# Optimization experiments

Hardware: AMD Instinct MI355X
Metric: run time of the kernel (lower is better)

Reference implementation:

```python
import jax, jax.numpy as jnp
import numpy as np

B, GEO_CH, SEM_CH, H, W = 8, 256, 256, 64, 64
HS, WS = 32, 32  # semantic branch spatial size
EPS_ATTN = 1e-6
EPS_GN = 1e-5


def _phi(x):
    return jax.nn.elu(x) + 1.0


def setup_inputs() -> dict:
    key = jax.random.key(0)
    ks = jax.random.split(key, 8)
    f_geo = jax.random.normal(ks[0], (B, GEO_CH, H, W), dtype=jnp.float32)
    f_sem = jax.random.normal(ks[1], (B, SEM_CH, HS, WS), dtype=jnp.float32)
    s = 0.02
    Wq = jax.random.normal(ks[2], (SEM_CH, GEO_CH), dtype=jnp.float32) * s
    Wk = jax.random.normal(ks[3], (SEM_CH, SEM_CH), dtype=jnp.float32) * s
    Wv = jax.random.normal(ks[4], (SEM_CH, SEM_CH), dtype=jnp.float32) * s
    Wo = jax.random.normal(ks[5], (GEO_CH, SEM_CH), dtype=jnp.float32) * s
    bq = jnp.zeros((SEM_CH,), jnp.float32)
    bk = jnp.zeros((SEM_CH,), jnp.float32)
    bv = jnp.zeros((SEM_CH,), jnp.float32)
    bo = jnp.zeros((GEO_CH,), jnp.float32)
    gn_w = jnp.ones((GEO_CH,), jnp.float32)
    gn_b = jnp.zeros((GEO_CH,), jnp.float32)
    return {"f_geo": f_geo, "f_sem": f_sem, "Wq": Wq, "bq": bq, "Wk": Wk,
            "bk": bk, "Wv": Wv, "bv": bv, "Wo": Wo, "bo": bo,
            "gn_w": gn_w, "gn_b": gn_b}


def _conv1x1(x, Wm, b):
    # x: [B,Cin,H,W], Wm: [Cout,Cin] -> [B,Cout,H,W]
    return jnp.einsum('oc,bchw->bohw', Wm, x) + b[None, :, None, None]


def reference(f_geo, f_sem, Wq, bq, Wk, bk, Wv, bv, Wo, bo, gn_w, gn_b):
    b, cg, h, w = f_geo.shape
    n = h * w
    # bilinear resize, half-pixel centers == torch align_corners=False
    f_sem_r = jax.image.resize(f_sem, (b, f_sem.shape[1], h, w), method='bilinear')
    Q = _phi(_conv1x1(f_geo, Wq, bq)).reshape(b, -1, n)      # [B,Cs,N]
    K = _phi(_conv1x1(f_sem_r, Wk, bk)).reshape(b, -1, n)    # [B,Cs,N]
    V = _conv1x1(f_sem_r, Wv, bv).reshape(b, -1, n)          # [B,Cs,N]
    KV = jnp.einsum('bcn,bdn->bcd', K, V)                    # [B,Cs,Cs]
    QKV = jnp.einsum('bcn,bcd->bnd', Q, KV)                  # [B,N,Cs]
    K_sum = K.sum(axis=-1)                                   # [B,Cs]
    norm = jnp.einsum('bcn,bc->bn', Q, K_sum)[..., None] + EPS_ATTN  # [B,N,1]
    out = (QKV / norm).transpose(0, 2, 1).reshape(b, -1, h, w)
    y = f_geo + _conv1x1(out, Wo, bo)
    # GroupNorm(1, geo_ch): normalize over (C,H,W) per sample, per-channel affine
    mu = y.mean(axis=(1, 2, 3), keepdims=True)
    var = y.var(axis=(1, 2, 3), keepdims=True)
    yn = (y - mu) * jax.lax.rsqrt(var + EPS_GN)
    return yn * gn_w[None, :, None, None] + gn_b[None, :, None, None]
```

## Files before the change

### kernel.cpp

```cpp
#include <hip/hip_runtime.h>
#include <hip/hip_bf16.h>


#define B_ 8
#define C_ 256
#define N_ 4096
#define NS_ 1024
#define KVCH 16

typedef unsigned short u16;
using bf16x8 = __attribute__((ext_vector_type(8))) short;
using f32x4 = __attribute__((ext_vector_type(4))) float;

__device__ inline u16 f2bf(float f) {
  unsigned u = __builtin_bit_cast(unsigned, f);
  unsigned r = (u + 0x7fffu + ((u >> 16) & 1u)) >> 16;
  return (u16)r;
}
__device__ inline float bf2f(u16 x) {
  return __builtin_bit_cast(float, ((unsigned)x) << 16);
}

__device__ __forceinline__ void gl_lds16(const u16* g, u16* l) {
  __builtin_amdgcn_global_load_lds((const __attribute__((address_space(1))) void*)g,
                                   (__attribute__((address_space(3))) void*)l, 16, 0, 0);
}

__device__ inline void gemm128_nt(const u16* __restrict__ At, const u16* __restrict__ Bt,
                                  int lda, int ldb, int k0, int k1,
                                  u16* __restrict__ lds, f32x4 acc[4][4])
{
  const int t = threadIdx.x;
  const int lane = t & 63, wave = t >> 6;
  const int wr = wave >> 1, wc = wave & 1;
  const int lr = lane & 15, lg = lane >> 4;
  const int sr = t >> 2, skv = (t & 3) * 8;
  u16* Ab = lds;
  u16* Bb = lds + 128 * 32;
  const u16* gA0 = At + (size_t)sr * lda + skv;
  const u16* gA1 = At + (size_t)(sr + 64) * lda + skv;
  const u16* gB0 = Bt + (size_t)sr * ldb + skv;
  const u16* gB1 = Bt + (size_t)(sr + 64) * ldb + skv;
  u16* dA0 = Ab + wave * 512;
  u16* dA1 = Ab + 2048 + wave * 512;
  u16* dB0 = Bb + wave * 512;
  u16* dB1 = Bb + 2048 + wave * 512;
  const u16* ap = Ab + (wr * 64 + lr) * 32 + lg * 8;
  const u16* bp = Bb + (wc * 64 + lr) * 32 + lg * 8;
  for (int k = k0; k < k1; k += 32) {
    gl_lds16(gA0 + k, dA0);
    gl_lds16(gA1 + k, dA1);
    gl_lds16(gB0 + k, dB0);
    gl_lds16(gB1 + k, dB1);
    __syncthreads();
    bf16x8 af[4], bfr[4];
#pragma unroll
    for (int i = 0; i < 4; ++i) af[i] = *reinterpret_cast<const bf16x8*>(ap + i * 16 * 32);
#pragma unroll
    for (int i = 0; i < 4; ++i) bfr[i] = *reinterpret_cast<const bf16x8*>(bp + i * 16 * 32);
#pragma unroll
    for (int m = 0; m < 4; ++m)
#pragma unroll
      for (int n = 0; n < 4; ++n)
        acc[m][n] = __builtin_amdgcn_mfma_f32_16x16x32_bf16(af[m], bfr[n], acc[m][n], 0, 0, 0);
    __syncthreads();
  }
}

__device__ inline void zero_acc(f32x4 acc[4][4]) {
#pragma unroll
  for (int m = 0; m < 4; ++m)
#pragma unroll
    for (int n = 0; n < 4; ++n)
#pragma unroll
      for (int r = 0; r < 4; ++r) acc[m][n][r] = 0.f;
}

__device__ inline void ep_stage_half(const f32x4 acc[4][4], float* eplds, int h,
                                     int wr, int wc, int lr, int lg)
{
  if (wr == h) {
#pragma unroll
    for (int m = 0; m < 4; ++m)
#pragma unroll
      for (int n = 0; n < 4; ++n)
#pragma unroll
        for (int r = 0; r < 4; ++r)
          eplds[(m * 16 + lg * 4 + r) * 132 + wc * 64 + n * 16 + lr] = acc[m][n][r];
  }
}

__global__ __launch_bounds__(256) void k_transpose_cast(const float* __restrict__ in,
                                                        u16* __restrict__ out, int rows, int cols)
{
  __shared__ float tile[32][33];
  int b = blockIdx.z;
  const float* src = in + (size_t)b * rows * cols;
  u16* dst = out + (size_t)b * rows * cols;
  int c0 = blockIdx.x * 32, r0 = blockIdx.y * 32;
  int tx = threadIdx.x & 31, ty = threadIdx.x >> 5;
#pragma unroll
  for (int i = 0; i < 32; i += 8)
    tile[ty + i][tx] = src[(size_t)(r0 + ty + i) * cols + (c0 + tx)];
  __syncthreads();
#pragma unroll
  for (int i = 0; i < 32; i += 8)
    dst[(size_t)(c0 + ty + i) * rows + (r0 + tx)] = f2bf(tile[tx][ty + i]);
}

__global__ __launch_bounds__(256) void k_cast4(const float* __restrict__ w0, const float* __restrict__ w1,
                                               const float* __restrict__ w2, const float* __restrict__ w3,
                                               u16* o0, u16* o1, u16* o2, u16* o3,
                                               float* __restrict__ stats, float* __restrict__ normv)
{
  int i = blockIdx.x * 256 + threadIdx.x;
  o0[i] = f2bf(w0[i]); o1[i] = f2bf(w1[i]); o2[i] = f2bf(w2[i]); o3[i] = f2bf(w3[i]);
  if (i < 16) stats[i] = 0.f;
  if (i < B_ * N_) normv[i] = 1e-6f;
}

__global__ __launch_bounds__(256) void k_semconv(const u16* __restrict__ fsemT,
                                                 const u16* __restrict__ Wk, const u16* __restrict__ Wv,
                                                 const float* __restrict__ bk, const float* __restrict__ bv,
                                                 u16* __restrict__ Kpre, u16* __restrict__ Vpre)
{
  __shared__ u16 glds[2 * 128 * 32];
  __shared__ float eplds[64 * 132];
  int b = blockIdx.z >> 1, sel = blockIdx.z & 1;
  int m0 = blockIdx.y * 128, n0 = blockIdx.x * 128;
  const u16* A = (sel ? Wv : Wk) + (size_t)m0 * C_;
  const u16* Bm = fsemT + (size_t)b * NS_ * C_ + (size_t)n0 * C_;
  const float* bias = sel ? bv : bk;
  u16* out = (sel ? Vpre : Kpre) + (size_t)b * C_ * NS_;
  f32x4 acc[4][4];
  zero_acc(acc);
  gemm128_nt(A, Bm, C_, C_, 0, C_, glds, acc);
  int t = threadIdx.x, lane = t & 63, wave = t >> 6;
  int wr = wave >> 1, wc = wave & 1, lr = lane & 15, lg = lane >> 4;
  for (int h = 0; h < 2; ++h) {
    __syncthreads();
    ep_stage_half(acc, eplds, h, wr, wc, lr, lg);
    __syncthreads();
#pragma unroll
    for (int it = 0; it < 8; ++it) {
      int rloc = it * 8 + (t >> 5), cloc = (t & 31) * 4;
      int row = m0 + h * 64 + rloc;
      float4 a = *(const float4*)&eplds[rloc * 132 + cloc];
      float bi = bias[row];
      ushort4 o;
      o.x = f2bf(a.x + bi); o.y = f2bf(a.y + bi); o.z = f2bf(a.z + bi); o.w = f2bf(a.w + bi);
      *(ushort4*)&out[(size_t)row * NS_ + n0 + cloc] = o;
    }
  }
}

__global__ __launch_bounds__(256) void k_resize(const u16* __restrict__ Kpre, const u16* __restrict__ Vpre,
                                                u16* __restrict__ Kbf, u16* __restrict__ Vbf,
                                                float* __restrict__ Ksum)
{
  int sel = blockIdx.y;
  const u16* src = (sel ? Vpre : Kpre) + (size_t)blockIdx.x * NS_;
  u16* dst = (sel ? Vbf : Kbf) + (size_t)blockIdx.x * N_;
  float s = 0.f;
  for (int i = threadIdx.x; i < N_; i += 256) {
    int yy = i >> 6, xx = i & 63;
    int yh = yy >> 1, xh = xx >> 1;
    int ys0, ys1, xs0, xs1; float wy0, wy1, wx0, wx1;
    if (yy & 1) { ys0 = yh; ys1 = yh < 31 ? yh + 1 : 31; wy0 = 0.75f; wy1 = 0.25f; }
    else        { ys0 = yh > 0 ? yh - 1 : 0; ys1 = yh;   wy0 = 0.25f; wy1 = 0.75f; }
    if (xx & 1) { xs0 = xh; xs1 = xh < 31 ? xh + 1 : 31; wx0 = 0.75f; wx1 = 0.25f; }
    else        { xs0 = xh > 0 ? xh - 1 : 0; xs1 = xh;   wx0 = 0.25f; wx1 = 0.75f; }
    float r0 = wx0 * bf2f(src[ys0 * 32 + xs0]) + wx1 * bf2f(src[ys0 * 32 + xs1]);
    float r1 = wx0 * bf2f(src[ys1 * 32 + xs0]) + wx1 * bf2f(src[ys1 * 32 + xs1]);
    float v = wy0 * r0 + wy1 * r1;
    if (!sel) { v = v > 0.f ? v + 1.f : __expf(v); s += v; }
    dst[i] = f2bf(v);
  }
  if (!sel) {
    __shared__ float red[256];
    red[threadIdx.x] = s; __syncthreads();
    for (int off = 128; off > 0; off >>= 1) {
      if (threadIdx.x < off) red[threadIdx.x] += red[threadIdx.x + off];
      __syncthreads();
    }
    if (threadIdx.x == 0) Ksum[blockIdx.x] = red[0];
  }
}

__global__ __launch_bounds__(256) void k_kv(const u16* __restrict__ Kbf, const u16* __restrict__ Vbf,
                                            float* __restrict__ KVpart)
{
  __shared__ u16 glds[2 * 128 * 32];
  __shared__ float eplds[64 * 132];
  int tn = blockIdx.x, tm = blockIdx.y;
  int b = blockIdx.z >> 4, ch = blockIdx.z & 15;
  const int kspan = N_ / KVCH;
  const u16* A = Kbf + (size_t)b * C_ * N_ + (size_t)tm * 128 * N_;
  const u16* Bm = Vbf + (size_t)b * C_ * N_ + (size_t)tn * 128 * N_;
  f32x4 acc[4][4];
  zero_acc(acc);
  gemm128_nt(A, Bm, N_, N_, ch * kspan, ch * kspan + kspan, glds, acc);
  float* out = KVpart + ((size_t)(b * KVCH + ch) * 4 + tm * 2 + tn) * (128 * 128);
  int t = threadIdx.x, lane = t & 63, wave = t >> 6;
  int wr = wave >> 1, wc = wave & 1, lr = lane & 15, lg = lane >> 4;
  for (int h = 0; h < 2; ++h) {
    __syncthreads();
    ep_stage_half(acc, eplds, h, wr, wc, lr, lg);
    __syncthreads();
#pragma unroll
    for (int it = 0; it < 8; ++it) {
      int rloc = it * 8 + (t >> 5), cloc = (t & 31) * 4;
      float4 a = *(const float4*)&eplds[rloc * 132 + cloc];
      *(float4*)&out[(size_t)(h * 64 + rloc) * 128 + cloc] = a;
    }
  }
}

__global__ __launch_bounds__(256) void k_kvred(const float* __restrict__ KVpart, u16* __restrict__ KVbf)
{
  int idx = blockIdx.x * 256 + threadIdx.x;
  int b = idx >> 16, cd = idx & 65535;
  int c = cd >> 8, d = cd & 255;
  int tile = (c >> 7) * 2 + (d >> 7);
  int loc = (c & 127) * 128 + (d & 127);
  float s = 0.f;
#pragma unroll
  for (int ch = 0; ch < KVCH; ++ch)
    s += KVpart[((size_t)(b * KVCH + ch) * 4 + tile) * 16384 + loc];
  KVbf[idx] = f2bf(s);
}

__global__ __launch_bounds__(256) void k_mgemm(const u16* __restrict__ Wo, const u16* __restrict__ KVbf,
                                               u16* __restrict__ Mbf)
{
  __shared__ u16 glds[2 * 128 * 32];
  __shared__ float eplds[64 * 132];
  int tn = blockIdx.x, tm = blockIdx.y, b = blockIdx.z;
  const u16* A = Wo + (size_t)tm * 128 * C_;
  const u16* Bm = KVbf + (size_t)b * C_ * C_ + (size_t)tn * 128 * C_;
  f32x4 acc[4][4];
  zero_acc(acc);
  gemm128_nt(A, Bm, C_, C_, 0, C_, glds, acc);
  u16* out = Mbf + (size_t)b * C_ * C_;
  int t = threadIdx.x, lane = t & 63, wave = t >> 6;
  int wr = wave >> 1, wc = wave & 1, lr = lane & 15, lg = lane >> 4;
  for (int h = 0; h < 2; ++h) {
    __syncthreads();
    ep_stage_half(acc, eplds, h, wr, wc, lr, lg);
    __syncthreads();
#pragma unroll
    for (int it = 0; it < 8; ++it) {
      int rloc = it * 8 + (t >> 5), cloc = (t & 31) * 4;
      int row = tm * 128 + h * 64 + rloc;
      float4 a = *(const float4*)&eplds[rloc * 132 + cloc];
      ushort4 o;
      o.x = f2bf(a.x); o.y = f2bf(a.y); o.z = f2bf(a.z); o.w = f2bf(a.w);
      *(ushort4*)&out[(size_t)row * C_ + tn * 128 + cloc] = o;
    }
  }
}

__global__ __launch_bounds__(256) void k_qgemm(const u16* __restrict__ fgeoT, const u16* __restrict__ Wq,
                                               const float* __restrict__ bq, const float* __restrict__ Ksum,
                                               u16* __restrict__ Qt, float* __restrict__ normv)
{
  __shared__ u16 glds[2 * 128 * 32];
  __shared__ float eplds[64 * 132];
  int tc = blockIdx.x, tn = blockIdx.y, b = blockIdx.z;
  const u16* A = fgeoT + (size_t)b * N_ * C_ + (size_t)tn * 128 * C_;
  const u16* Bm = Wq + (size_t)tc * 128 * C_;
  f32x4 acc[4][4];
  zero_acc(acc);
  gemm128_nt(A, Bm, C_, C_, 0, C_, glds, acc);
  u16* out = Qt + (size_t)b * N_ * C_;
  float* nb = normv + (size_t)b * N_;
  int t = threadIdx.x, lane = t & 63, wave = t >> 6;
  int wr = wave >> 1, wc = wave & 1, lr = lane & 15, lg = lane >> 4;
  for (int h = 0; h < 2; ++h) {
    __syncthreads();
    ep_stage_half(acc, eplds, h, wr, wc, lr, lg);
    __syncthreads();
#pragma unroll
    for (int it = 0; it < 8; ++it) {
      int rloc = it * 8 + (t >> 5), cloc = (t & 31) * 4;
      int row = tn * 128 + h * 64 + rloc;
      int col = tc * 128 + cloc;
      float4 a = *(const float4*)&eplds[rloc * 132 + cloc];
      float4 bqv = *(const float4*)&bq[col];
      float4 ks = *(const float4*)&Ksum[b * C_ + col];
      float v0 = a.x + bqv.x; v0 = v0 > 0.f ? v0 + 1.f : __expf(v0);
      float v1 = a.y + bqv.y; v1 = v1 > 0.f ? v1 + 1.f : __expf(v1);
      float v2 = a.z + bqv.z; v2 = v2 > 0.f ? v2 + 1.f : __expf(v2);
      float v3 = a.w + bqv.w; v3 = v3 > 0.f ? v3 + 1.f : __expf(v3);
      ushort4 o;
      o.x = f2bf(v0); o.y = f2bf(v1); o.z = f2bf(v2); o.w = f2bf(v3);
      *(ushort4*)&out[(size_t)row * C_ + col] = o;
      float p = v0 * ks.x + v1 * ks.y + v2 * ks.z + v3 * ks.w;
      p += __shfl_xor(p, 1); p += __shfl_xor(p, 2);
      p += __shfl_xor(p, 4); p += __shfl_xor(p, 8); p += __shfl_xor(p, 16);
      if ((t & 31) == 0) atomicAdd(&nb[row], p);
    }
  }
}

__global__ __launch_bounds__(256) void k_final(const u16* __restrict__ Mbf, const u16* __restrict__ Qt,
                                               const float* __restrict__ fgeo, const float* __restrict__ bo,
                                               const float* __restrict__ normv,
                                               float* __restrict__ y, float* __restrict__ stats)
{
  __shared__ u16 glds[2 * 128 * 32];
  __shared__ float eplds[64 * 132];
  int tn = blockIdx.x, tm = blockIdx.y, b = blockIdx.z;
  const u16* A = Mbf + (size_t)b * C_ * C_ + (size_t)tm * 128 * C_;
  const u16* Bm = Qt + (size_t)b * N_ * C_ + (size_t)tn * 128 * C_;
  f32x4 acc[4][4];
  zero_acc(acc);
  gemm128_nt(A, Bm, C_, C_, 0, C_, glds, acc);
  const float* nrm = normv + (size_t)b * N_;
  const float* fg = fgeo + (size_t)b * C_ * N_;
  float* yb = y + (size_t)b * C_ * N_;
  int t = threadIdx.x, lane = t & 63, wave = t >> 6;
  int wr = wave >> 1, wc = wave & 1, lr = lane & 15, lg = lane >> 4;
  float ssum = 0.f, ssq = 0.f;
  for (int h = 0; h < 2; ++h) {
    __syncthreads();
    ep_stage_half(acc, eplds, h, wr, wc, lr, lg);
    __syncthreads();
#pragma unroll
    for (int it = 0; it < 8; ++it) {
      int rloc = it * 8 + (t >> 5), cloc = (t & 31) * 4;
      int row = tm * 128 + h * 64 + rloc;
      int col = tn * 128 + cloc;
      float4 a = *(const float4*)&eplds[rloc * 132 + cloc];
      float4 nv = *(const float4*)&nrm[col];
      float4 f = *(const float4*)&fg[(size_t)row * N_ + col];
      float bov = bo[row];
      float4 v;
      v.x = f.x + bov + a.x / nv.x;
      v.y = f.y + bov + a.y / nv.y;
      v.z = f.z + bov + a.z / nv.z;
      v.w = f.w + bov + a.w / nv.w;
      *(float4*)&yb[(size_t)row * N_ + col] = v;
      ssum += v.x + v.y + v.z + v.w;
      ssq += v.x * v.x + v.y * v.y + v.z * v.z + v.w * v.w;
    }
  }
#pragma unroll
  for (int off = 1; off < 64; off <<= 1) {
    ssum += __shfl_xor(ssum, off);
    ssq += __shfl_xor(ssq, off);
  }
  if (lane == 0) {
    atomicAdd(&stats[b * 2], ssum);
    atomicAdd(&stats[b * 2 + 1], ssq);
  }
}

__global__ __launch_bounds__(256) void k_gn(float* __restrict__ y, const float* __restrict__ stats,
                                            const float* __restrict__ gnw, const float* __restrict__ gnb)
{
  int idx = blockIdx.x * 256 + threadIdx.x;
  int elem = idx * 8;
  int b = elem >> 20;
  int o = (elem >> 12) & 255;
  const float cnt = (float)C_ * (float)N_;
  float mu = stats[b * 2] / cnt;
  float var = stats[b * 2 + 1] / cnt - mu * mu;
  float rs = rsqrtf(var + 1e-5f);
  float sc = gnw[o] * rs;
  float sh = gnb[o] - mu * sc;
  float4* p = reinterpret_cast<float4*>(y) + idx * 2;
  float4 v0 = p[0], v1 = p[1];
  v0.x = v0.x * sc + sh; v0.y = v0.y * sc + sh; v0.z = v0.z * sc + sh; v0.w = v0.w * sc + sh;
  v1.x = v1.x * sc + sh; v1.y = v1.y * sc + sh; v1.z = v1.z * sc + sh; v1.w = v1.w * sc + sh;
  p[0] = v0; p[1] = v1;
}

extern "C" void kernel_launch(void* const* d_in, const int* in_sizes, int n_in,
                              void* d_out, int out_size, void* d_ws, size_t ws_size,
                              hipStream_t stream)
{
  const float* f_geo = (const float*)d_in[0];
  const float* f_sem = (const float*)d_in[1];
  const float* Wq = (const float*)d_in[2];
  const float* bq = (const float*)d_in[3];
  const float* Wk = (const float*)d_in[4];
  const float* bk = (const float*)d_in[5];
  const float* Wv = (const float*)d_in[6];
  const float* bv = (const float*)d_in[7];
  const float* Wo = (const float*)d_in[8];
  const float* bo = (const float*)d_in[9];
  const float* gnw = (const float*)d_in[10];
  const float* gnb = (const float*)d_in[11];
  float* y = (float*)d_out;

  char* w = (char*)d_ws;
  auto alloc = [&](size_t bytes) { char* p = w; w += (bytes + 255) & ~(size_t)255; return p; };
  u16* fsemT = (u16*)alloc((size_t)B_ * NS_ * C_ * 2);
  u16* fgeoT = (u16*)alloc((size_t)B_ * N_ * C_ * 2);
  u16* Wqb = (u16*)alloc(65536 * 2);
  u16* Wkb = (u16*)alloc(65536 * 2);
  u16* Wvb = (u16*)alloc(65536 * 2);
  u16* Wob = (u16*)alloc(65536 * 2);
  u16* Kpre = (u16*)alloc((size_t)B_ * C_ * NS_ * 2);
  u16* Vpre = (u16*)alloc((size_t)B_ * C_ * NS_ * 2);
  u16* Kbf = (u16*)alloc((size_t)B_ * C_ * N_ * 2);
  u16* Vbf = (u16*)alloc((size_t)B_ * C_ * N_ * 2);
  float* Ksum = (float*)alloc((size_t)B_ * C_ * 4);
  float* KVpart = (float*)alloc((size_t)B_ * KVCH * 4 * 16384 * 4);
  u16* KVbf = (u16*)alloc((size_t)B_ * C_ * C_ * 2);
  u16* Mbf = (u16*)alloc((size_t)B_ * C_ * C_ * 2);
  u16* Qt = (u16*)alloc((size_t)B_ * N_ * C_ * 2);
  float* normv = (float*)alloc((size_t)B_ * N_ * 4);
  float* stats = (float*)alloc(256);

  k_transpose_cast<<<dim3(NS_ / 32, C_ / 32, B_), 256, 0, stream>>>(f_sem, fsemT, C_, NS_);
  k_transpose_cast<<<dim3(N_ / 32, C_ / 32, B_), 256, 0, stream>>>(f_geo, fgeoT, C_, N_);
  k_cast4<<<dim3(256), 256, 0, stream>>>(Wq, Wk, Wv, Wo, Wqb, Wkb, Wvb, Wob, stats, normv);
  k_semconv<<<dim3(8, 2, 16), 256, 0, stream>>>(fsemT, Wkb, Wvb, bk, bv, Kpre, Vpre);
  k_resize<<<dim3(B_ * C_, 2), 256, 0, stream>>>(Kpre, Vpre, Kbf, Vbf, Ksum);
  k_kv<<<dim3(2, 2, B_ * KVCH), 256, 0, stream>>>(Kbf, Vbf, KVpart);
  k_kvred<<<dim3(2048), 256, 0, stream>>>(KVpart, KVbf);
  k_mgemm<<<dim3(2, 2, B_), 256, 0, stream>>>(Wob, KVbf, Mbf);
  k_qgemm<<<dim3(2, 32, B_), 256, 0, stream>>>(fgeoT, Wqb, bq, Ksum, Qt, normv);
  k_final<<<dim3(32, 2, B_), 256, 0, stream>>>(Mbf, Qt, f_geo, bo, normv, y, stats);
  k_gn<<<dim3(B_ * C_ * N_ / 8 / 256), 256, 0, stream>>>(y, stats, gnw, gnb);
}
```

Baseline: 266.1 us.

## Double-buffer GEMM K-loop, shrink tiles, store KV partials in bf16

Generalizes the shared GEMM helper into a templated double-buffered version, so the global-to-LDS load of the next K-slice is issued before the current slice's MFMAs. It also aliases staging and epilogue LDS and stages the epilogue in 32-row chunks. The Q-projection and final GEMMs move to 64-wide tiles to double the block count. The KV split-K count doubles, and partials are written as bf16 and reduced with vectorized loads. This raises parallelism and cuts partial-buffer traffic, at the cost of extra rounding on the KV partials and more epilogue barriers.

```diff
diff --git a/kernel.cpp b/kernel.cpp
--- a/kernel.cpp
+++ b/kernel.cpp
@@ -6,7 +6,7 @@
 #define C_ 256
 #define N_ 4096
 #define NS_ 1024
-#define KVCH 16
+#define KVCH 32
 
 typedef unsigned short u16;
 using bf16x8 = __attribute__((ext_vector_type(8))) short;
@@ -26,67 +26,78 @@
                                    (__attribute__((address_space(3))) void*)l, 16, 0, 0);
 }
 
-__device__ inline void gemm128_nt(const u16* __restrict__ At, const u16* __restrict__ Bt,
-                                  int lda, int ldb, int k0, int k1,
-                                  u16* __restrict__ lds, f32x4 acc[4][4])
+template<int FM, int FN>
+__device__ inline void zero_acc(f32x4 (&acc)[FM][FN]) {
+#pragma unroll
+  for (int m = 0; m < FM; ++m)
+#pragma unroll
+    for (int n = 0; n < FN; ++n)
+#pragma unroll
+      for (int r = 0; r < 4; ++r) acc[m][n][r] = 0.f;
+}
+
+template<int TM, int TN>
+__device__ inline void gemm_nt(const u16* __restrict__ At, const u16* __restrict__ Bt,
+                               int lda, int ldb, int k0, int k1,
+                               u16* __restrict__ lds, f32x4 (&acc)[TM/32][TN/32])
 {
   const int t = threadIdx.x;
   const int lane = t & 63, wave = t >> 6;
   const int wr = wave >> 1, wc = wave & 1;
   const int lr = lane & 15, lg = lane >> 4;
   const int sr = t >> 2, skv = (t & 3) * 8;
-  u16* Ab = lds;
-  u16* Bb = lds + 128 * 32;
-  const u16* gA0 = At + (size_t)sr * lda + skv;
-  const u16* gA1 = At + (size_t)(sr + 64) * lda + skv;
-  const u16* gB0 = Bt + (size_t)sr * ldb + skv;
-  const u16* gB1 = Bt + (size_t)(sr + 64) * ldb + skv;
-  u16* dA0 = Ab + wave * 512;
-  u16* dA1 = Ab + 2048 + wave * 512;
-  u16* dB0 = Bb + wave * 512;
-  u16* dB1 = Bb + 2048 + wave * 512;
-  const u16* ap = Ab + (wr * 64 + lr) * 32 + lg * 8;
-  const u16* bp = Bb + (wc * 64 + lr) * 32 + lg * 8;
-  for (int k = k0; k < k1; k += 32) {
-    gl_lds16(gA0 + k, dA0);
-    gl_lds16(gA1 + k, dA1);
-    gl_lds16(gB0 + k, dB0);
-    gl_lds16(gB1 + k, dB1);
-    __syncthreads();
-    bf16x8 af[4], bfr[4];
-#pragma unroll
-    for (int i = 0; i < 4; ++i) af[i] = *reinterpret_cast<const bf16x8*>(ap + i * 16 * 32);
-#pragma unroll
-    for (int i = 0; i < 4; ++i) bfr[i] = *reinterpret_cast<const bf16x8*>(bp + i * 16 * 32);
-#pragma unroll
-    for (int m = 0; m < 4; ++m)
-#pragma unroll
-      for (int n = 0; n < 4; ++n)
+  constexpr int BUF = (TM + TN) * 32;
+  const u16* gA = At + (size_t)sr * lda + skv;
+  const u16* gB = Bt + (size_t)sr * ldb + skv;
+  auto stage = [&](int buf, int k) {
+    u16* Ab = lds + buf * BUF;
+    u16* Bb = Ab + TM * 32;
+#pragma unroll
+    for (int i = 0; i < TM / 64; ++i)
+      gl_lds16(gA + (size_t)i * 64 * lda + k, Ab + i * 2048 + wave * 512);
+#pragma unroll
+    for (int i = 0; i < TN / 64; ++i)
+      gl_lds16(gB + (size_t)i * 64 * ldb + k, Bb + i * 2048 + wave * 512);
+  };
+  stage(0, k0);
+  __syncthreads();
+  const int nt = (k1 - k0) >> 5;
+  int cur = 0;
+  for (int it = 0; it < nt; ++it) {
+    if (it + 1 < nt) stage(cur ^ 1, k0 + (it + 1) * 32);
+    const u16* Ab = lds + cur * BUF;
+    const u16* Bb = Ab + TM * 32;
+    const u16* ap = Ab + (wr * (TM / 2) + lr) * 32 + lg * 8;
+    const u16* bp = Bb + (wc * (TN / 2) + lr) * 32 + lg * 8;
+    bf16x8 af[TM / 32], bfr[TN / 32];
+#pragma unroll
+    for (int i = 0; i < TM / 32; ++i) af[i] = *(const bf16x8*)(ap + i * 16 * 32);
+#pragma unroll
+    for (int i = 0; i < TN / 32; ++i) bfr[i] = *(const bf16x8*)(bp + i * 16 * 32);
+#pragma unroll
+    for (int m = 0; m < TM / 32; ++m)
+#pragma unroll
+      for (int n = 0; n < TN / 32; ++n)
         acc[m][n] = __builtin_amdgcn_mfma_f32_16x16x32_bf16(af[m], bfr[n], acc[m][n], 0, 0, 0);
     __syncthreads();
-  }
-}
-
-__device__ inline void zero_acc(f32x4 acc[4][4]) {
-#pragma unroll
-  for (int m = 0; m < 4; ++m)
-#pragma unroll
-    for (int n = 0; n < 4; ++n)
-#pragma unroll
-      for (int r = 0; r < 4; ++r) acc[m][n][r] = 0.f;
-}
-
-__device__ inline void ep_stage_half(const f32x4 acc[4][4], float* eplds, int h,
-                                     int wr, int wc, int lr, int lg)
-{
-  if (wr == h) {
-#pragma unroll
-    for (int m = 0; m < 4; ++m)
-#pragma unroll
-      for (int n = 0; n < 4; ++n)
+    cur ^= 1;
+  }
+}
+
+template<int TM, int TN>
+__device__ inline void ep_stage_chunk(const f32x4 (&acc)[TM/32][TN/32], float* eplds, int q,
+                                      int wr, int wc, int lr, int lg)
+{
+#pragma unroll
+  for (int m = 0; m < TM / 32; ++m) {
+    int r0 = wr * (TM / 2) + m * 16;
+    if (r0 >= q * 32 && r0 < q * 32 + 32) {
+#pragma unroll
+      for (int n = 0; n < TN / 32; ++n)
 #pragma unroll
         for (int r = 0; r < 4; ++r)
-          eplds[(m * 16 + lg * 4 + r) * 132 + wc * 64 + n * 16 + lr] = acc[m][n][r];
+          eplds[(r0 - q * 32 + lg * 4 + r) * (TN + 4) + wc * (TN / 2) + n * 16 + lr] = acc[m][n][r];
+    }
   }
 }
 
@@ -124,8 +135,9 @@
                                                  const float* __restrict__ bk, const float* __restrict__ bv,
                                                  u16* __restrict__ Kpre, u16* __restrict__ Vpre)
 {
-  __shared__ u16 glds[2 * 128 * 32];
-  __shared__ float eplds[64 * 132];
+  __shared__ __align__(16) char smem[32768];
+  u16* glds = (u16*)smem;
+  float* eplds = (float*)smem;
   int b = blockIdx.z >> 1, sel = blockIdx.z & 1;
   int m0 = blockIdx.y * 128, n0 = blockIdx.x * 128;
   const u16* A = (sel ? Wv : Wk) + (size_t)m0 * C_;
@@ -134,23 +146,23 @@
   u16* out = (sel ? Vpre : Kpre) + (size_t)b * C_ * NS_;
   f32x4 acc[4][4];
   zero_acc(acc);
-  gemm128_nt(A, Bm, C_, C_, 0, C_, glds, acc);
+  gemm_nt<128, 128>(A, Bm, C_, C_, 0, C_, glds, acc);
   int t = threadIdx.x, lane = t & 63, wave = t >> 6;
   int wr = wave >> 1, wc = wave & 1, lr = lane & 15, lg = lane >> 4;
-  for (int h = 0; h < 2; ++h) {
-    __syncthreads();
-    ep_stage_half(acc, eplds, h, wr, wc, lr, lg);
-    __syncthreads();
-#pragma unroll
-    for (int it = 0; it < 8; ++it) {
-      int rloc = it * 8 + (t >> 5), cloc = (t & 31) * 4;
-      int row = m0 + h * 64 + rloc;
+  for (int q = 0; q < 4; ++q) {
+    ep_stage_chunk<128, 128>(acc, eplds, q, wr, wc, lr, lg);
+    __syncthreads();
+#pragma unroll
+    for (int p = 0; p < 4; ++p) {
+      int rloc = p * 8 + (t >> 5), cloc = (t & 31) * 4;
+      int row = m0 + q * 32 + rloc;
       float4 a = *(const float4*)&eplds[rloc * 132 + cloc];
       float bi = bias[row];
       ushort4 o;
       o.x = f2bf(a.x + bi); o.y = f2bf(a.y + bi); o.z = f2bf(a.z + bi); o.w = f2bf(a.w + bi);
       *(ushort4*)&out[(size_t)row * NS_ + n0 + cloc] = o;
     }
+    __syncthreads();
   }
 }
 
@@ -188,75 +200,86 @@
 }
 
 __global__ __launch_bounds__(256) void k_kv(const u16* __restrict__ Kbf, const u16* __restrict__ Vbf,
-                                            float* __restrict__ KVpart)
-{
-  __shared__ u16 glds[2 * 128 * 32];
-  __shared__ float eplds[64 * 132];
+                                            u16* __restrict__ KVpart)
+{
+  __shared__ __align__(16) char smem[32768];
+  u16* glds = (u16*)smem;
+  float* eplds = (float*)smem;
   int tn = blockIdx.x, tm = blockIdx.y;
-  int b = blockIdx.z >> 4, ch = blockIdx.z & 15;
+  int b = blockIdx.z >> 5, ch = blockIdx.z & 31;
   const int kspan = N_ / KVCH;
   const u16* A = Kbf + (size_t)b * C_ * N_ + (size_t)tm * 128 * N_;
   const u16* Bm = Vbf + (size_t)b * C_ * N_ + (size_t)tn * 128 * N_;
   f32x4 acc[4][4];
   zero_acc(acc);
-  gemm128_nt(A, Bm, N_, N_, ch * kspan, ch * kspan + kspan, glds, acc);
-  float* out = KVpart + ((size_t)(b * KVCH + ch) * 4 + tm * 2 + tn) * (128 * 128);
+  gemm_nt<128, 128>(A, Bm, N_, N_, ch * kspan, ch * kspan + kspan, glds, acc);
+  u16* out = KVpart + ((size_t)(b * KVCH + ch) * 4 + tm * 2 + tn) * (128 * 128);
   int t = threadIdx.x, lane = t & 63, wave = t >> 6;
   int wr = wave >> 1, wc = wave & 1, lr = lane & 15, lg = lane >> 4;
-  for (int h = 0; h < 2; ++h) {
-    __syncthreads();
-    ep_stage_half(acc, eplds, h, wr, wc, lr, lg);
-    __syncthreads();
-#pragma unroll
-    for (int it = 0; it < 8; ++it) {
-      int rloc = it * 8 + (t >> 5), cloc = (t & 31) * 4;
+  for (int q = 0; q < 4; ++q) {
+    ep_stage_chunk<128, 128>(acc, eplds, q, wr, wc, lr, lg);
+    __syncthreads();
+#pragma unroll
+    for (int p = 0; p < 4; ++p) {
+      int rloc = p * 8 + (t >> 5), cloc = (t & 31) * 4;
       float4 a = *(const float4*)&eplds[rloc * 132 + cloc];
-      *(float4*)&out[(size_t)(h * 64 + rloc) * 128 + cloc] = a;
-    }
-  }
-}
-
-__global__ __launch_bounds__(256) void k_kvred(const float* __restrict__ KVpart, u16* __restrict__ KVbf)
-{
-  int idx = blockIdx.x * 256 + threadIdx.x;
-  int b = idx >> 16, cd = idx & 65535;
-  int c = cd >> 8, d = cd & 255;
-  int tile = (c >> 7) * 2 + (d >> 7);
-  int loc = (c & 127) * 128 + (d & 127);
-  float s = 0.f;
-#pragma unroll
-  for (int ch = 0; ch < KVCH; ++ch)
-    s += KVpart[((size_t)(b * KVCH + ch) * 4 + tile) * 16384 + loc];
-  KVbf[idx] = f2bf(s);
+      ushort4 o;
+      o.x = f2bf(a.x); o.y = f2bf(a.y); o.z = f2bf(a.z); o.w = f2bf(a.w);
+      *(ushort4*)&out[(size_t)(q * 32 + rloc) * 128 + cloc] = o;
+    }
+    __syncthreads();
+  }
+}
+
+__global__ __launch_bounds__(256) void k_kvred(const u16* __restrict__ KVpart, u16* __restrict__ KVbf)
+{
+  int q = blockIdx.x * 256 + threadIdx.x;
+  int b = q >> 14;
+  int rem = q & 16383;
+  int c = rem >> 6;
+  int d0 = (rem & 63) * 4;
+  int tile = ((c >> 7) << 1) + (d0 >> 7);
+  int loc = (c & 127) * 128 + (d0 & 127);
+  const u16* base = KVpart + (size_t)b * KVCH * 4 * 16384 + (size_t)tile * 16384 + loc;
+  float s0 = 0.f, s1 = 0.f, s2 = 0.f, s3 = 0.f;
+#pragma unroll
+  for (int ch = 0; ch < KVCH; ++ch) {
+    ushort4 v = *(const ushort4*)(base + (size_t)ch * 4 * 16384);
+    s0 += bf2f(v.x); s1 += bf2f(v.y); s2 += bf2f(v.z); s3 += bf2f(v.w);
+  }
+  ushort4 o;
+  o.x = f2bf(s0); o.y = f2bf(s1); o.z = f2bf(s2); o.w = f2bf(s3);
+  *(ushort4*)&KVbf[(size_t)q * 4] = o;
 }
 
 __global__ __launch_bounds__(256) void k_mgemm(const u16* __restrict__ Wo, const u16* __restrict__ KVbf,
                                                u16* __restrict__ Mbf)
 {
-  __shared__ u16 glds[2 * 128 * 32];
-  __shared__ float eplds[64 * 132];
+  __shared__ __align__(16) char smem[32768];
+  u16* glds = (u16*)smem;
+  float* eplds = (float*)smem;
   int tn = blockIdx.x, tm = blockIdx.y, b = blockIdx.z;
   const u16* A = Wo + (size_t)tm * 128 * C_;
   const u16* Bm = KVbf + (size_t)b * C_ * C_ + (size_t)tn * 128 * C_;
   f32x4 acc[4][4];
   zero_acc(acc);
-  gemm128_nt(A, Bm, C_, C_, 0, C_, glds, acc);
+  gemm_nt<128, 128>(A, Bm, C_, C_, 0, C_, glds, acc);
   u16* out = Mbf + (size_t)b * C_ * C_;
   int t = threadIdx.x, lane = t & 63, wave = t >> 6;
   int wr = wave >> 1, wc = wave & 1, lr = lane & 15, lg = lane >> 4;
-  for (int h = 0; h < 2; ++h) {
-    __syncthreads();
-    ep_stage_half(acc, eplds, h, wr, wc, lr, lg);
-    __syncthreads();
-#pragma unroll
-    for (int it = 0; it < 8; ++it) {
-      int rloc = it * 8 + (t >> 5), cloc = (t & 31) * 4;
-      int row = tm * 128 + h * 64 + rloc;
+  for (int q = 0; q < 4; ++q) {
+    ep_stage_chunk<128, 128>(acc, eplds, q, wr, wc, lr, lg);
+    __syncthreads();
+#pragma unroll
+    for (int p = 0; p < 4; ++p) {
+      int rloc = p * 8 + (t >> 5), cloc = (t & 31) * 4;
+      int row = tm * 128 + q * 32 + rloc;
       float4 a = *(const float4*)&eplds[rloc * 132 + cloc];
       ushort4 o;
       o.x = f2bf(a.x); o.y = f2bf(a.y); o.z = f2bf(a.z); o.w = f2bf(a.w);
       *(ushort4*)&out[(size_t)row * C_ + tn * 128 + cloc] = o;
     }
+    __syncthreads();
   }
 }
 
@@ -264,26 +287,26 @@
                                                const float* __restrict__ bq, const float* __restrict__ Ksum,
                                                u16* __restrict__ Qt, float* __restrict__ normv)
 {
-  __shared__ u16 glds[2 * 128 * 32];
-  __shared__ float eplds[64 * 132];
+  __shared__ __align__(16) char smem[24576];
+  u16* glds = (u16*)smem;
+  float* eplds = (float*)smem;
   int tc = blockIdx.x, tn = blockIdx.y, b = blockIdx.z;
-  const u16* A = fgeoT + (size_t)b * N_ * C_ + (size_t)tn * 128 * C_;
+  const u16* A = fgeoT + (size_t)b * N_ * C_ + (size_t)tn * 64 * C_;
   const u16* Bm = Wq + (size_t)tc * 128 * C_;
-  f32x4 acc[4][4];
+  f32x4 acc[2][4];
   zero_acc(acc);
-  gemm128_nt(A, Bm, C_, C_, 0, C_, glds, acc);
+  gemm_nt<64, 128>(A, Bm, C_, C_, 0, C_, glds, acc);
   u16* out = Qt + (size_t)b * N_ * C_;
   float* nb = normv + (size_t)b * N_;
   int t = threadIdx.x, lane = t & 63, wave = t >> 6;
   int wr = wave >> 1, wc = wave & 1, lr = lane & 15, lg = lane >> 4;
-  for (int h = 0; h < 2; ++h) {
-    __syncthreads();
-    ep_stage_half(acc, eplds, h, wr, wc, lr, lg);
-    __syncthreads();
-#pragma unroll
-    for (int it = 0; it < 8; ++it) {
-      int rloc = it * 8 + (t >> 5), cloc = (t & 31) * 4;
-      int row = tn * 128 + h * 64 + rloc;
+  for (int q = 0; q < 2; ++q) {
+    ep_stage_chunk<64, 128>(acc, eplds, q, wr, wc, lr, lg);
+    __syncthreads();
+#pragma unroll
+    for (int p = 0; p < 4; ++p) {
+      int rloc = p * 8 + (t >> 5), cloc = (t & 31) * 4;
+      int row = tn * 64 + q * 32 + rloc;
       int col = tc * 128 + cloc;
       float4 a = *(const float4*)&eplds[rloc * 132 + cloc];
       float4 bqv = *(const float4*)&bq[col];
@@ -295,11 +318,12 @@
       ushort4 o;
       o.x = f2bf(v0); o.y = f2bf(v1); o.z = f2bf(v2); o.w = f2bf(v3);
       *(ushort4*)&out[(size_t)row * C_ + col] = o;
-      float p = v0 * ks.x + v1 * ks.y + v2 * ks.z + v3 * ks.w;
-      p += __shfl_xor(p, 1); p += __shfl_xor(p, 2);
-      p += __shfl_xor(p, 4); p += __shfl_xor(p, 8); p += __shfl_xor(p, 16);
-      if ((t & 31) == 0) atomicAdd(&nb[row], p);
-    }
+      float pv = v0 * ks.x + v1 * ks.y + v2 * ks.z + v3 * ks.w;
+      pv += __shfl_xor(pv, 1); pv += __shfl_xor(pv, 2);
+      pv += __shfl_xor(pv, 4); pv += __shfl_xor(pv, 8); pv += __shfl_xor(pv, 16);
+      if ((t & 31) == 0) atomicAdd(&nb[row], pv);
+    }
+    __syncthreads();
   }
 }
 
@@ -308,30 +332,30 @@
                                                const float* __restrict__ normv,
                                                float* __restrict__ y, float* __restrict__ stats)
 {
-  __shared__ u16 glds[2 * 128 * 32];
-  __shared__ float eplds[64 * 132];
+  __shared__ __align__(16) char smem[24576];
+  u16* glds = (u16*)smem;
+  float* eplds = (float*)smem;
   int tn = blockIdx.x, tm = blockIdx.y, b = blockIdx.z;
   const u16* A = Mbf + (size_t)b * C_ * C_ + (size_t)tm * 128 * C_;
-  const u16* Bm = Qt + (size_t)b * N_ * C_ + (size_t)tn * 128 * C_;
-  f32x4 acc[4][4];
+  const u16* Bm = Qt + (size_t)b * N_ * C_ + (size_t)tn * 64 * C_;
+  f32x4 acc[4][2];
   zero_acc(acc);
-  gemm128_nt(A, Bm, C_, C_, 0, C_, glds, acc);
+  gemm_nt<128, 64>(A, Bm, C_, C_, 0, C_, glds, acc);
   const float* nrm = normv + (size_t)b * N_;
   const float* fg = fgeo + (size_t)b * C_ * N_;
   float* yb = y + (size_t)b * C_ * N_;
   int t = threadIdx.x, lane = t & 63, wave = t >> 6;
   int wr = wave >> 1, wc = wave & 1, lr = lane & 15, lg = lane >> 4;
   float ssum = 0.f, ssq = 0.f;
-  for (int h = 0; h < 2; ++h) {
-    __syncthreads();
-    ep_stage_half(acc, eplds, h, wr, wc, lr, lg);
-    __syncthreads();
-#pragma unroll
-    for (int it = 0; it < 8; ++it) {
-      int rloc = it * 8 + (t >> 5), cloc = (t & 31) * 4;
-      int row = tm * 128 + h * 64 + rloc;
-      int col = tn * 128 + cloc;
-      float4 a = *(const float4*)&eplds[rloc * 132 + cloc];
+  for (int q = 0; q < 4; ++q) {
+    ep_stage_chunk<128, 64>(acc, eplds, q, wr, wc, lr, lg);
+    __syncthreads();
+#pragma unroll
+    for (int p = 0; p < 2; ++p) {
+      int rloc = p * 16 + (t >> 4), cloc = (t & 15) * 4;
+      int row = tm * 128 + q * 32 + rloc;
+      int col = tn * 64 + cloc;
+      float4 a = *(const float4*)&eplds[rloc * 68 + cloc];
       float4 nv = *(const float4*)&nrm[col];
       float4 f = *(const float4*)&fg[(size_t)row * N_ + col];
       float bov = bo[row];
@@ -344,6 +368,7 @@
       ssum += v.x + v.y + v.z + v.w;
       ssq += v.x * v.x + v.y * v.y + v.z * v.z + v.w * v.w;
     }
+    __syncthreads();
   }
 #pragma unroll
   for (int off = 1; off < 64; off <<= 1) {
@@ -407,7 +432,7 @@
   u16* Kbf = (u16*)alloc((size_t)B_ * C_ * N_ * 2);
   u16* Vbf = (u16*)alloc((size_t)B_ * C_ * N_ * 2);
   float* Ksum = (float*)alloc((size_t)B_ * C_ * 4);
-  float* KVpart = (float*)alloc((size_t)B_ * KVCH * 4 * 16384 * 4);
+  u16* KVpart = (u16*)alloc((size_t)B_ * KVCH * 4 * 16384 * 2);
   u16* KVbf = (u16*)alloc((size_t)B_ * C_ * C_ * 2);
   u16* Mbf = (u16*)alloc((size_t)B_ * C_ * C_ * 2);
   u16* Qt = (u16*)alloc((size_t)B_ * N_ * C_ * 2);
@@ -420,9 +445,9 @@
   k_semconv<<<dim3(8, 2, 16), 256, 0, stream>>>(fsemT, Wkb, Wvb, bk, bv, Kpre, Vpre);
   k_resize<<<dim3(B_ * C_, 2), 256, 0, stream>>>(Kpre, Vpre, Kbf, Vbf, Ksum);
   k_kv<<<dim3(2, 2, B_ * KVCH), 256, 0, stream>>>(Kbf, Vbf, KVpart);
-  k_kvred<<<dim3(2048), 256, 0, stream>>>(KVpart, KVbf);
+  k_kvred<<<dim3(512), 256, 0, stream>>>(KVpart, KVbf);
   k_mgemm<<<dim3(2, 2, B_), 256, 0, stream>>>(Wob, KVbf, Mbf);
-  k_qgemm<<<dim3(2, 32, B_), 256, 0, stream>>>(fgeoT, Wqb, bq, Ksum, Qt, normv);
-  k_final<<<dim3(32, 2, B_), 256, 0, stream>>>(Mbf, Qt, f_geo, bo, normv, y, stats);
+  k_qgemm<<<dim3(2, 64, B_), 256, 0, stream>>>(fgeoT, Wqb, bq, Ksum, Qt, normv);
+  k_final<<<dim3(64, 2, B_), 256, 0, stream>>>(Mbf, Qt, f_geo, bo, normv, y, stats);
   k_gn<<<dim3(B_ * C_ * N_ / 8 / 256), 256, 0, stream>>>(y, stats, gnw, gnb);
 }
```

Measured after the change: 321.2 us. 20.7% more time.
